# Performance work log

Hardware: AMD Instinct MI355X
Metric: run time of the kernel (lower is better)

Reference implementation:

```python
import jax, jax.numpy as jnp
import numpy as np

EPS_RMS = 1e-6
EPS_SCALE = 1e-5


def setup_inputs() -> dict:
    key = jax.random.key(0)
    k1, k2 = jax.random.split(key)
    B, S, D_IN, D_OUT = 4, 2048, 2048, 8192
    x = jax.random.normal(k1, (B, S, D_IN), dtype=jnp.float32)
    # kaiming_uniform-ish init bound
    bound = 1.0 / np.sqrt(D_IN)
    weight = jax.random.uniform(k2, (D_OUT, D_IN), dtype=jnp.float32, minval=-bound, maxval=bound)
    gamma = jnp.ones((D_IN,), dtype=jnp.float32)
    return {"x": x, "weight": weight, "gamma": gamma}


def rmsnorm(x, gamma):
    xf = x.astype(jnp.float32)
    inv = jax.lax.rsqrt(jnp.mean(xf * xf, axis=-1, keepdims=True) + EPS_RMS)
    return (xf * inv).astype(x.dtype) * gamma


def quantize_weights_ternary(weight):
    scale = jnp.maximum(jnp.mean(jnp.abs(weight)), EPS_SCALE)
    wn = weight / scale
    wq = jax.lax.stop_gradient(jnp.round(jnp.clip(wn, -1.0, 1.0)) - wn) + wn  # STE
    return wq, scale


def reference(x, weight, gamma):
    x_norm = rmsnorm(x, gamma)                      # [B, S, D_in]
    wq, scale = quantize_weights_ternary(weight)    # [D_out, D_in], scalar
    out = jnp.einsum('bsd,od->bso', x_norm, wq)     # [B, S, D_out]
    return out * scale
```

## Files before the change

kernel.cpp:

```cpp
#include <hip/hip_runtime.h>
#include <hip/hip_bf16.h>
#include <stdint.h>

#define M_ROWS 8192
#define K_DIM  2048
#define N_DIM  8192
#define W_ELEMS (N_DIM * K_DIM)
#define X_ELEMS (M_ROWS * K_DIM)
#define NT 32
#define ABSUM_BLOCKS 256

typedef __bf16 v8bf __attribute__((ext_vector_type(8)));
typedef float  v4f  __attribute__((ext_vector_type(4)));

__device__ inline unsigned short f2bf(float f) {
  uint32_t u = __builtin_bit_cast(uint32_t, f);
  uint32_t r = (u + 0x7fffu + ((u >> 16) & 1u)) >> 16;
  return (unsigned short)r;
}

__device__ inline void async_copy16(const void* g, void* l) {
  __builtin_amdgcn_global_load_lds(
      (const __attribute__((address_space(1))) void*)g,
      (__attribute__((address_space(3))) void*)l, 16, 0, 0);
}

__global__ __launch_bounds__(256) void prep_kernel(const float* __restrict__ X,
                                                   const float* __restrict__ gamma,
                                                   const float* __restrict__ W,
                                                   unsigned short* __restrict__ Xn,
                                                   double* __restrict__ partials) {
  __shared__ double wsumd[4];
  __shared__ float wsumf[4];
  const int t = threadIdx.x;
  const int lane = t & 63, wid = t >> 6;

  if (blockIdx.x < ABSUM_BLOCKS) {
    const int pb = blockIdx.x;
    int tid = pb * 256 + t;
    const float4* W4 = (const float4*)W;
    const int n4 = W_ELEMS / 4;
    double acc = 0.0;
    for (int i = tid; i < n4; i += ABSUM_BLOCKS * 256) {
      float4 v = W4[i];
      acc += (double)fabsf(v.x) + (double)fabsf(v.y) +
             (double)fabsf(v.z) + (double)fabsf(v.w);
    }
    for (int off = 32; off > 0; off >>= 1) acc += __shfl_down(acc, off);
    if (lane == 0) wsumd[wid] = acc;
    __syncthreads();
    if (t == 0) partials[pb] = wsumd[0] + wsumd[1] + wsumd[2] + wsumd[3];
    return;
  }

  const int row = blockIdx.x - ABSUM_BLOCKS;
  const float4* xr = (const float4*)(X + (size_t)row * K_DIM);
  float4 a = xr[t];
  float4 b = xr[t + 256];
  float ss = a.x * a.x + a.y * a.y + a.z * a.z + a.w * a.w +
             b.x * b.x + b.y * b.y + b.z * b.z + b.w * b.w;
  for (int off = 32; off > 0; off >>= 1) ss += __shfl_down(ss, off);
  if (lane == 0) wsumf[wid] = ss;
  __syncthreads();
  float total = wsumf[0] + wsumf[1] + wsumf[2] + wsumf[3];
  float inv = 1.0f / sqrtf(total * (1.0f / (float)K_DIM) + 1e-6f);
  const float4* gr = (const float4*)gamma;
  float4 g0 = gr[t];
  float4 g1 = gr[t + 256];
  union { unsigned short h[4]; uint2 u; } pa, pb;
  pa.h[0] = f2bf((a.x * inv) * g0.x);
  pa.h[1] = f2bf((a.y * inv) * g0.y);
  pa.h[2] = f2bf((a.z * inv) * g0.z);
  pa.h[3] = f2bf((a.w * inv) * g0.w);
  pb.h[0] = f2bf((b.x * inv) * g1.x);
  pb.h[1] = f2bf((b.y * inv) * g1.y);
  pb.h[2] = f2bf((b.z * inv) * g1.z);
  pb.h[3] = f2bf((b.w * inv) * g1.w);
  uint2* orow = (uint2*)(Xn + (size_t)row * K_DIM);
  orow[t] = pa.u;
  orow[t + 256] = pb.u;
}

__global__ __launch_bounds__(256) void reduce_kernel(const double* __restrict__ partials,
                                                     float* __restrict__ scale) {
  double v = partials[threadIdx.x];
  for (int off = 32; off > 0; off >>= 1) v += __shfl_down(v, off);
  __shared__ double ws[4];
  int lane = threadIdx.x & 63, wid = threadIdx.x >> 6;
  if (lane == 0) ws[wid] = v;
  __syncthreads();
  if (threadIdx.x == 0) {
    double total = ws[0] + ws[1] + ws[2] + ws[3];
    scale[0] = (float)fmax(total * (1.0 / (double)W_ELEMS), 1e-5);
  }
}

__global__ __launch_bounds__(256) void quant_kernel(const float* __restrict__ W,
                                                    const float* __restrict__ scale,
                                                    unsigned short* __restrict__ Wq) {
  float s = scale[0];
  const int t = threadIdx.x;
  const float4* W4 = (const float4*)W + (size_t)blockIdx.x * 512;
  float4 a = W4[t];
  float4 b = W4[t + 256];
  union { unsigned short h[4]; uint2 u; } pa, pb;
  pa.h[0] = f2bf(rintf(fminf(1.f, fmaxf(-1.f, a.x / s))));
  pa.h[1] = f2bf(rintf(fminf(1.f, fmaxf(-1.f, a.y / s))));
  pa.h[2] = f2bf(rintf(fminf(1.f, fmaxf(-1.f, a.z / s))));
  pa.h[3] = f2bf(rintf(fminf(1.f, fmaxf(-1.f, a.w / s))));
  pb.h[0] = f2bf(rintf(fminf(1.f, fmaxf(-1.f, b.x / s))));
  pb.h[1] = f2bf(rintf(fminf(1.f, fmaxf(-1.f, b.y / s))));
  pb.h[2] = f2bf(rintf(fminf(1.f, fmaxf(-1.f, b.z / s))));
  pb.h[3] = f2bf(rintf(fminf(1.f, fmaxf(-1.f, b.w / s))));
  uint2* o = (uint2*)(Wq + (size_t)blockIdx.x * 2048);
  o[t] = pa.u;
  o[t + 256] = pb.u;
}

__global__ __launch_bounds__(512, 2) void gemm_kernel(
    const unsigned short* __restrict__ A,
    const unsigned short* __restrict__ B,
    const float* __restrict__ scale,
    float* __restrict__ C) {
  __shared__ __align__(16) char lds[131072];

  const int tid = threadIdx.x;
  const int lane = tid & 63;
  const int wave = tid >> 6;
  const int wm = wave & 1;
  const int wn = wave >> 1;

  const int bid = blockIdx.x;
  const int xcd = bid & 7;
  const int idx = bid >> 3;
  const int half = idx >> 6;
  const int i6 = idx & 63;
  const int mb = xcd * 2 + half * 16 + ((i6 >> 2) & 1);
  const int nb = (i6 >> 3) * 4 + (i6 & 3);
  const int m0 = mb * 256;
  const int n0 = nb * 256;

  const int srow3 = lane >> 3;
  const int scg = (lane & 7) ^ srow3;

  const int aoff_a = wm * 8192 + (lane & 15) * 128;
  const int boff_b = wn * 4096 + (lane & 15) * 128;
  const int swzk0 = ((lane >> 4) ^ (lane & 7)) << 4;
  const int swzk1 = ((4 + (lane >> 4)) ^ (lane & 7)) << 4;

  v4f acc[8][4] = {};
  v8bf af[4][2];
  v8bf b0f[2][2];
  v8bf b1f[2][2];

#define STAGE_A(B_, H_, KT_) do {                                              \
    _Pragma("unroll")                                                          \
    for (int j = 0; j < 2; ++j) {                                              \
      const int chunk_ = wave * 2 + j;                                         \
      const int slot_ = chunk_ * 8 + srow3;                                    \
      const int row_ = ((slot_ >> 6) << 7) + ((H_) << 6) + (slot_ & 63);       \
      async_copy16(A + (size_t)(m0 + row_) * K_DIM + ((KT_) << 6) + (scg << 3),\
                   lds + (B_) * 32768 + (H_) * 16384 + chunk_ * 1024);         \
    } } while (0)

#define STAGE_B(B_, H_, KT_) do {                                              \
    _Pragma("unroll")                                                          \
    for (int j = 0; j < 2; ++j) {                                              \
      const int chunk_ = wave * 2 + j;                                         \
      const int slot_ = chunk_ * 8 + srow3;                                    \
      const int row_ = ((slot_ >> 5) << 6) + ((H_) << 5) + (slot_ & 31);       \
      async_copy16(B + (size_t)(n0 + row_) * K_DIM + ((KT_) << 6) + (scg << 3),\
                   lds + 65536 + (B_) * 32768 + (H_) * 16384 + chunk_ * 1024); \
    } } while (0)

#define LOADA(B_, QM_) do {                                                    \
    _Pragma("unroll")                                                          \
    for (int tm = 0; tm < 4; ++tm) {                                           \
      af[tm][0] = *(const v8bf*)(lds + (B_) * 32768 + (QM_) * 16384 +          \
                                 aoff_a + tm * 2048 + swzk0);                  \
      af[tm][1] = *(const v8bf*)(lds + (B_) * 32768 + (QM_) * 16384 +          \
                                 aoff_a + tm * 2048 + swzk1);                  \
    } } while (0)

#define LOADB(B_, QN_, DST) do {                                               \
    _Pragma("unroll")                                                          \
    for (int tn = 0; tn < 2; ++tn) {                                           \
      DST[tn][0] = *(const v8bf*)(lds + 65536 + (B_) * 32768 + (QN_) * 16384 + \
                                  boff_b + tn * 2048 + swzk0);                 \
      DST[tn][1] = *(const v8bf*)(lds + 65536 + (B_) * 32768 + (QN_) * 16384 + \
                                  boff_b + tn * 2048 + swzk1);                 \
    } } while (0)

#define MMAC(BF, QM_, QN_) do {                                                \
    _Pragma("unroll")                                                          \
    for (int ks = 0; ks < 2; ++ks)                                             \
    _Pragma("unroll")                                                          \
    for (int tm = 0; tm < 4; ++tm)                                             \
    _Pragma("unroll")                                                          \
    for (int tn = 0; tn < 2; ++tn)                                             \
      acc[(QM_) * 4 + tm][(QN_) * 2 + tn] =                                    \
          __builtin_amdgcn_mfma_f32_16x16x32_bf16(                             \
              BF[tn][ks], af[tm][ks],                                          \
              acc[(QM_) * 4 + tm][(QN_) * 2 + tn], 0, 0, 0);                   \
  } while (0)

#define BARRIER() __builtin_amdgcn_s_barrier()
#define VM8() asm volatile("s_waitcnt vmcnt(8)" ::: "memory")

#define TILE(T_, B_) do {                                                      \
    const int t1_ = ((T_) + 1 < NT) ? (T_) + 1 : NT - 1;                       \
    const int t2_ = ((T_) + 2 < NT) ? (T_) + 2 : NT - 1;                       \
               \
    LOADA(B_, 0);                                                              \
    STAGE_A(1 - (B_), 1, t1_);                                                 \
    BARRIER();                                                                 \
    __builtin_amdgcn_s_setprio(1); MMAC(b0f, 0, 0);                            \
    __builtin_amdgcn_s_setprio(0);                                             \
    BARRIER();                                                                 \
                                                            \
    LOADB(B_, 1, b1f);                                                         \
    BARRIER();                                                                 \
    __builtin_amdgcn_s_setprio(1); MMAC(b1f, 0, 1);                            \
    __builtin_amdgcn_s_setprio(0);                                             \
    VM8(); BARRIER();                                                          \
                                                            \
    LOADA(B_, 1);                                                              \
    STAGE_A(B_, 0, t2_);                                                       \
    STAGE_B(B_, 1, t2_);                                                       \
    BARRIER();                                                                 \
    __builtin_amdgcn_s_setprio(1); MMAC(b0f, 1, 0);                            \
    __builtin_amdgcn_s_setprio(0);                                             \
    BARRIER();                                                                 \
                             \
    STAGE_B(B_, 0, t2_);                                                       \
    VM8(); BARRIER();                                                          \
    LOADB(1 - (B_), 0, b0f);                                                   \
    __builtin_amdgcn_s_setprio(1); MMAC(b1f, 1, 1);                            \
    __builtin_amdgcn_s_setprio(0);                                             \
    BARRIER();                                                                 \
  } while (0)

  STAGE_A(0, 0, 0);
  STAGE_B(0, 0, 0);
  STAGE_B(0, 1, 0);
  STAGE_A(0, 1, 0);
  STAGE_A(1, 0, 1);
  STAGE_B(1, 1, 1);
  STAGE_B(1, 0, 1);
  VM8();
  BARRIER();
  LOADB(0, 0, b0f);

  for (int t = 0; t < NT; t += 2) {
    TILE(t, 0);
    TILE(t + 1, 1);
  }

  const float s = scale[0];
  const int mBase = m0 + wm * 128 + (lane & 15);
  const int nBase = n0 + wn * 64 + ((lane >> 4) << 2);
#pragma unroll
  for (int tm = 0; tm < 8; ++tm) {
#pragma unroll
    for (int tn = 0; tn < 4; ++tn) {
      v4f v = acc[tm][tn] * s;
      __builtin_nontemporal_store(
          v, (v4f*)&C[(size_t)(mBase + tm * 16) * N_DIM + (nBase + tn * 16)]);
    }
  }

#undef STAGE_A
#undef STAGE_B
#undef LOADA
#undef LOADB
#undef MMAC
#undef BARRIER
#undef VM8
#undef TILE
}

extern "C" void kernel_launch(void* const* d_in, const int* in_sizes, int n_in,
                              void* d_out, int out_size, void* d_ws, size_t ws_size,
                              hipStream_t stream) {
  const float* x = (const float*)d_in[0];
  const float* w = (const float*)d_in[1];
  const float* gamma = (const float*)d_in[2];
  float* out = (float*)d_out;

  float* scale_f = (float*)d_ws;
  unsigned short* xn = (unsigned short*)((char*)d_ws + 16);
  unsigned short* wq = (unsigned short*)((char*)d_ws + 16 + (size_t)X_ELEMS * 2);
  double* partials = (double*)wq;

  prep_kernel<<<ABSUM_BLOCKS + M_ROWS, 256, 0, stream>>>(x, gamma, w, xn, partials);
  reduce_kernel<<<1, 256, 0, stream>>>(partials, scale_f);
  quant_kernel<<<W_ELEMS / 2048, 256, 0, stream>>>(w, scale_f, wq);
  gemm_kernel<<<(M_ROWS / 256) * (N_DIM / 256), 512, 0, stream>>>(xn, wq, scale_f, out);
}
```

Before: 605.6 us.

## Fuse scale reduction into quant, cut GEMM barriers, remap tile order

Drops the single-block reduce kernel: every quant block now reduces the 256 double partials itself, and block 0 writes the scale for the GEMM. Partials move into the output buffer so they no longer share space with Wq. In the GEMM main loop most s_barriers are removed, leaving two combined vmcnt(8)+barrier points per tile, and the last MFMA group is moved ahead of the second sync. The block-to-tile swizzle is changed for L2 locality and stores become regular instead of nontemporal. Fewer barriers risk LDS read/write races, and every quant block now repeats the redundant partial reduction.

```diff
diff --git a/kernel.cpp b/kernel.cpp
--- a/kernel.cpp
+++ b/kernel.cpp
@@ -23,6 +23,15 @@
   __builtin_amdgcn_global_load_lds(
       (const __attribute__((address_space(1))) void*)g,
       (__attribute__((address_space(3))) void*)l, 16, 0, 0);
+}
+
+__device__ inline float scale_from_partials(const double* __restrict__ partials) {
+  const int lane = threadIdx.x & 63;
+  double d = partials[lane] + partials[lane + 64] +
+             partials[lane + 128] + partials[lane + 192];
+  for (int off = 32; off > 0; off >>= 1) d += __shfl_down(d, off);
+  d = __shfl(d, 0);
+  return (float)fmax(d * (1.0 / (double)W_ELEMS), 1e-5);
 }
 
 __global__ __launch_bounds__(256) void prep_kernel(const float* __restrict__ X,
@@ -81,25 +90,13 @@
   orow[t + 256] = pb.u;
 }
 
-__global__ __launch_bounds__(256) void reduce_kernel(const double* __restrict__ partials,
-                                                     float* __restrict__ scale) {
-  double v = partials[threadIdx.x];
-  for (int off = 32; off > 0; off >>= 1) v += __shfl_down(v, off);
-  __shared__ double ws[4];
-  int lane = threadIdx.x & 63, wid = threadIdx.x >> 6;
-  if (lane == 0) ws[wid] = v;
-  __syncthreads();
-  if (threadIdx.x == 0) {
-    double total = ws[0] + ws[1] + ws[2] + ws[3];
-    scale[0] = (float)fmax(total * (1.0 / (double)W_ELEMS), 1e-5);
-  }
-}
-
 __global__ __launch_bounds__(256) void quant_kernel(const float* __restrict__ W,
-                                                    const float* __restrict__ scale,
+                                                    const double* __restrict__ partials,
+                                                    float* __restrict__ scale_out,
                                                     unsigned short* __restrict__ Wq) {
-  float s = scale[0];
+  const float s = scale_from_partials(partials);
   const int t = threadIdx.x;
+  if (blockIdx.x == 0 && t == 0) scale_out[0] = s;
   const float4* W4 = (const float4*)W + (size_t)blockIdx.x * 512;
   float4 a = W4[t];
   float4 b = W4[t + 256];
@@ -131,12 +128,10 @@
   const int wn = wave >> 1;
 
   const int bid = blockIdx.x;
-  const int xcd = bid & 7;
-  const int idx = bid >> 3;
-  const int half = idx >> 6;
-  const int i6 = idx & 63;
-  const int mb = xcd * 2 + half * 16 + ((i6 >> 2) & 1);
-  const int nb = (i6 >> 3) * 4 + (i6 & 3);
+  const int swz = (bid & 7) * 128 + (bid >> 3);
+  const int st = swz >> 4, wi = swz & 15;
+  const int mb = (st >> 3) * 4 + (wi >> 2);
+  const int nb = (st & 7) * 4 + (wi & 3);
   const int m0 = mb * 256;
   const int n0 = nb * 256;
 
@@ -204,40 +199,38 @@
               acc[(QM_) * 4 + tm][(QN_) * 2 + tn], 0, 0, 0);                   \
   } while (0)
 
-#define BARRIER() __builtin_amdgcn_s_barrier()
-#define VM8() asm volatile("s_waitcnt vmcnt(8)" ::: "memory")
+#define SYNC8() do {                                                           \
+    asm volatile("s_waitcnt vmcnt(8)" ::: "memory");                           \
+    __builtin_amdgcn_s_barrier();                                              \
+    asm volatile("" ::: "memory");                                             \
+    __builtin_amdgcn_sched_barrier(0);                                         \
+  } while (0)
 
 #define TILE(T_, B_) do {                                                      \
     const int t1_ = ((T_) + 1 < NT) ? (T_) + 1 : NT - 1;                       \
     const int t2_ = ((T_) + 2 < NT) ? (T_) + 2 : NT - 1;                       \
-               \
+                                  \
     LOADA(B_, 0);                                                              \
     STAGE_A(1 - (B_), 1, t1_);                                                 \
-    BARRIER();                                                                 \
     __builtin_amdgcn_s_setprio(1); MMAC(b0f, 0, 0);                            \
     __builtin_amdgcn_s_setprio(0);                                             \
-    BARRIER();                                                                 \
                                                             \
     LOADB(B_, 1, b1f);                                                         \
-    BARRIER();                                                                 \
     __builtin_amdgcn_s_setprio(1); MMAC(b1f, 0, 1);                            \
     __builtin_amdgcn_s_setprio(0);                                             \
-    VM8(); BARRIER();                                                          \
+    SYNC8();                                                                   \
                                                             \
     LOADA(B_, 1);                                                              \
     STAGE_A(B_, 0, t2_);                                                       \
     STAGE_B(B_, 1, t2_);                                                       \
-    BARRIER();                                                                 \
     __builtin_amdgcn_s_setprio(1); MMAC(b0f, 1, 0);                            \
     __builtin_amdgcn_s_setprio(0);                                             \
-    BARRIER();                                                                 \
-                             \
+                                                            \
     STAGE_B(B_, 0, t2_);                                                       \
-    VM8(); BARRIER();                                                          \
+    __builtin_amdgcn_s_setprio(1); MMAC(b1f, 1, 1);                            \
+    __builtin_amdgcn_s_setprio(0);                                             \
+    SYNC8();                                                                   \
     LOADB(1 - (B_), 0, b0f);                                                   \
-    __builtin_amdgcn_s_setprio(1); MMAC(b1f, 1, 1);                            \
-    __builtin_amdgcn_s_setprio(0);                                             \
-    BARRIER();                                                                 \
   } while (0)
 
   STAGE_A(0, 0, 0);
@@ -247,8 +240,7 @@
   STAGE_A(1, 0, 1);
   STAGE_B(1, 1, 1);
   STAGE_B(1, 0, 1);
-  VM8();
-  BARRIER();
+  SYNC8();
   LOADB(0, 0, b0f);
 
   for (int t = 0; t < NT; t += 2) {
@@ -263,9 +255,12 @@
   for (int tm = 0; tm < 8; ++tm) {
 #pragma unroll
     for (int tn = 0; tn < 4; ++tn) {
-      v4f v = acc[tm][tn] * s;
-      __builtin_nontemporal_store(
-          v, (v4f*)&C[(size_t)(mBase + tm * 16) * N_DIM + (nBase + tn * 16)]);
+      float4 v;
+      v.x = acc[tm][tn][0] * s;
+      v.y = acc[tm][tn][1] * s;
+      v.z = acc[tm][tn][2] * s;
+      v.w = acc[tm][tn][3] * s;
+      *(float4*)&C[(size_t)(mBase + tm * 16) * N_DIM + (nBase + tn * 16)] = v;
     }
   }
 
@@ -274,8 +269,7 @@
 #undef LOADA
 #undef LOADB
 #undef MMAC
-#undef BARRIER
-#undef VM8
+#undef SYNC8
 #undef TILE
 }
 
@@ -290,10 +284,9 @@
   float* scale_f = (float*)d_ws;
   unsigned short* xn = (unsigned short*)((char*)d_ws + 16);
   unsigned short* wq = (unsigned short*)((char*)d_ws + 16 + (size_t)X_ELEMS * 2);
-  double* partials = (double*)wq;
+  double* partials = (double*)out;
 
   prep_kernel<<<ABSUM_BLOCKS + M_ROWS, 256, 0, stream>>>(x, gamma, w, xn, partials);
-  reduce_kernel<<<1, 256, 0, stream>>>(partials, scale_f);
-  quant_kernel<<<W_ELEMS / 2048, 256, 0, stream>>>(w, scale_f, wq);
+  quant_kernel<<<W_ELEMS / 2048, 256, 0, stream>>>(w, partials, scale_f, wq);
   gemm_kernel<<<(M_ROWS / 256) * (N_DIM / 256), 512, 0, stream>>>(xn, wq, scale_f, out);
 }
```

Result: no change. 611.2 us (+0.9%).
